# Optimization experiments

Hardware: AMD Instinct MI355X
Metric: run time of the kernel (lower is better)

Reference implementation:

```python
import jax, jax.numpy as jnp
import numpy as np

T, N, E, P, D, F = 24, 10000, 320000, 20000, 64, 32


def setup_inputs() -> dict:
    key = jax.random.key(0)
    ks = jax.random.split(key, 16)
    s = 0.05

    def nrm(k, shape):
        return jax.random.normal(k, shape, jnp.float32) * s

    return {
        "x": jax.random.normal(ks[0], (T, N, F + 2), jnp.float32),
        "dis": jax.random.uniform(ks[1], (N, N), dtype=jnp.float32),
        "src": jax.random.randint(ks[2], (E,), 0, N, jnp.int32),
        "dst": jax.random.randint(ks[3], (E,), 0, N, jnp.int32),
        "train_idx": jax.random.randint(ks[4], (2, P), 0, N, jnp.int32),
        "ru_W1": nrm(ks[5], (D + F, D)), "ru_b1": jnp.zeros((D,), jnp.float32),
        "ru_W2": nrm(ks[6], (D, D)), "ru_b2": jnp.zeros((D,), jnp.float32),
        "ru_W3": nrm(ks[7], (D, 2 * D)), "ru_b3": jnp.zeros((2 * D,), jnp.float32),
        "rh_W1": nrm(ks[8], (D + F, D)), "rh_b1": jnp.zeros((D,), jnp.float32),
        "rh_W2": nrm(ks[9], (D, D)), "rh_b2": jnp.zeros((D,), jnp.float32),
        "rh_W3": nrm(ks[10], (D, D)), "rh_b3": jnp.zeros((D,), jnp.float32),
        "pred_W": nrm(ks[11], (2 * D + 1, 1)), "pred_b": jnp.zeros((1,), jnp.float32),
    }


def reference(x, dis, src, dst, train_idx,
              ru_W1, ru_b1, ru_W2, ru_b2, ru_W3, ru_b3,
              rh_W1, rh_b1, rh_W2, rh_b2, rh_W3, rh_b3,
              pred_W, pred_b):
    # DGL GraphConv, norm='both': h <- D_in^{-1/2} A D_out^{-1/2} h W + b (deg clamped to >=1)
    ones = jnp.ones((E,), jnp.float32)
    out_norm = jax.lax.rsqrt(jnp.maximum(jax.ops.segment_sum(ones, src, num_segments=N), 1.0))
    in_norm = jax.lax.rsqrt(jnp.maximum(jax.ops.segment_sum(ones, dst, num_segments=N), 1.0))

    def gconv(h, W, b):
        m = (h * out_norm[:, None])[src]                              # gather [E, d]
        agg = jax.ops.segment_sum(m, dst, num_segments=N) * in_norm[:, None]
        return agg @ W + b

    def gnn(h, W1, b1, W2, b2, W3, b3):
        h = jax.nn.relu(gconv(h, W1, b1))
        h = jax.nn.relu(gconv(h, W2, b2))
        return gconv(h, W3, b3)

    feat = x[:, :, :-2]                                               # [T, N, F]

    def step(h, xt):
        ru = jax.nn.sigmoid(gnn(jnp.concatenate([h, xt], -1),
                                ru_W1, ru_b1, ru_W2, ru_b2, ru_W3, ru_b3))
        r, z = ru[:, :D], ru[:, D:]
        h_new = jnp.tanh(gnn(jnp.concatenate([h * r, xt], -1),
                             rh_W1, rh_b1, rh_W2, rh_b2, rh_W3, rh_b3))
        h = z * h + (1.0 - z) * h_new
        return h, h

    _, hs = jax.lax.scan(step, jnp.zeros((N, D), x.dtype), feat)      # [T, N, D]

    ori = hs[:, train_idx[0]]                                         # [T, P, D]
    dst_e = hs[:, train_idx[1]]                                       # [T, P, D]
    d = jnp.broadcast_to(dis[train_idx[0], train_idx[1]][None, :, None], (T, P, 1))
    flow = jnp.tanh(jnp.concatenate([ori, dst_e, d], -1) @ pred_W + pred_b)  # [T, P, 1]
    return flow[:, :, 0].T                                            # [P, T]
```

## Files before the change

kernel.cpp:

```cpp
#include <hip/hip_runtime.h>
#include <cstdint>
#include <cstddef>

#define T_ 24
#define N_ 10000
#define E_ 320000
#define P_ 20000
#define D_ 64
#define F_ 32
#define XS_ 34
#define NZROWS 64

#define SCOPE_AGENT __HIP_MEMORY_SCOPE_AGENT

typedef float f32x4 __attribute__((ext_vector_type(4)));

__device__ __forceinline__ float ldsc(const float* p) {
  return __hip_atomic_load((const float*)p, __ATOMIC_RELAXED, SCOPE_AGENT);
}
__device__ __forceinline__ float2 ldsc2(const float* p) {
  unsigned long long u =
      __hip_atomic_load((const unsigned long long*)p, __ATOMIC_RELAXED, SCOPE_AGENT);
  float2 r;
  r.x = __uint_as_float((unsigned)(u & 0xffffffffu));
  r.y = __uint_as_float((unsigned)(u >> 32));
  return r;
}
__device__ __forceinline__ void stsc(float* p, float v) {
  __hip_atomic_store(p, v, __ATOMIC_RELAXED, SCOPE_AGENT);
}
__device__ __forceinline__ void stsc16(float* p, f32x4 v) {
  asm volatile("global_store_dwordx4 %0, %1, off sc1" :: "v"(p), "v"(v) : "memory");
}
__device__ __forceinline__ f32x4 ld4sc(const float* p) {
  f32x4 v;
  asm volatile("global_load_dwordx4 %0, %1, off sc1" : "=v"(v) : "v"(p));
  return v;
}
__device__ __forceinline__ void vmwait0() {
  asm volatile("s_waitcnt vmcnt(0)" ::: "memory");
  __builtin_amdgcn_sched_barrier(0);
}


__global__ void deg_kernel(const int* __restrict__ src, const int* __restrict__ dst,
                           int* __restrict__ deg_out, int* __restrict__ deg_in) {
  int e = blockIdx.x * blockDim.x + threadIdx.x;
  if (e < E_) {
    atomicAdd(&deg_out[src[e]], 1);
    atomicAdd(&deg_in[dst[e]], 1);
  }
}

__global__ void norm_kernel(const int* __restrict__ deg_in, const int* __restrict__ deg_out,
                            float* __restrict__ in_norm, float* __restrict__ out_norm) {
  int n = blockIdx.x * blockDim.x + threadIdx.x;
  if (n < N_) {
    in_norm[n]  = 1.0f / sqrtf(fmaxf((float)deg_in[n], 1.0f));
    out_norm[n] = 1.0f / sqrtf(fmaxf((float)deg_out[n], 1.0f));
  }
}

__global__ __launch_bounds__(1024) void scan_kernel(const int* __restrict__ deg,
                                                    int* __restrict__ row_ptr) {
  __shared__ int buf[1024];
  __shared__ int carry;
  int tid = threadIdx.x;
  if (tid == 0) { carry = 0; row_ptr[0] = 0; }
  __syncthreads();
  for (int base = 0; base < N_; base += 1024) {
    int i = base + tid;
    int v = (i < N_) ? deg[i] : 0;
    buf[tid] = v;
    __syncthreads();
    for (int off = 1; off < 1024; off <<= 1) {
      int tv = (tid >= off) ? buf[tid - off] : 0;
      __syncthreads();
      buf[tid] += tv;
      __syncthreads();
    }
    if (i < N_) row_ptr[i + 1] = carry + buf[tid];
    __syncthreads();
    if (tid == 0) carry += buf[1023];
    __syncthreads();
  }
}

__global__ void fill_kernel(const int* __restrict__ src, const int* __restrict__ dst,
                            const int* __restrict__ row_ptr, int* __restrict__ fill,
                            int* __restrict__ col) {
  int e = blockIdx.x * blockDim.x + threadIdx.x;
  if (e < E_) {
    int n = dst[e];
    int pos = row_ptr[n] + atomicAdd(&fill[n], 1);
    col[pos] = src[e];
  }
}

__global__ void dvec_kernel(const float* __restrict__ dis, const int* __restrict__ ti,
                            float* __restrict__ dvec) {
  int p = blockIdx.x * blockDim.x + threadIdx.x;
  if (p < P_) {
    int i0 = ti[p];
    int i1 = ti[P_ + p];
    dvec[p] = dis[(size_t)i0 * N_ + i1];
  }
}


struct Args {
  const float* x;
  const int* row_ptr;
  const int* col;
  const float* in_norm;
  const float* out_norm;
  const float* ruW1; const float* ruB1;
  const float* ruW2; const float* ruB2;
  const float* ruW3; const float* ruB3;
  const float* rhW1; const float* rhB1;
  const float* rhW2; const float* rhB2;
  const float* rhW3; const float* rhB3;
  const float* pW; const float* pb;
  const int* ti; const float* dvec;
  float* h; float* z; float* tA; float* tB;
  float* out;
  unsigned* slots;
  unsigned* epoch;
};

__device__ __forceinline__ void gbar(const Args& A, unsigned nblk, unsigned& ep) {
  __syncthreads();
  ++ep;
  const int tid = threadIdx.x;
  if (blockIdx.x == 0) {
    if (tid > 0 && tid < (int)nblk) {
      while (__hip_atomic_load(&A.slots[tid], __ATOMIC_RELAXED, SCOPE_AGENT) < ep)
        __builtin_amdgcn_s_sleep(2);
    }
    __syncthreads();
    if (tid == 0)
      __hip_atomic_store(A.epoch, ep, __ATOMIC_RELAXED, SCOPE_AGENT);
  } else {
    if (tid == 0) {
      __hip_atomic_store(&A.slots[blockIdx.x], ep, __ATOMIC_RELAXED, SCOPE_AGENT);
      while (__hip_atomic_load(A.epoch, __ATOMIC_RELAXED, SCOPE_AGENT) < ep)
        __builtin_amdgcn_s_sleep(2);
    }
    __syncthreads();
  }
}

__device__ __forceinline__ void stageW(const float* __restrict__ W, int n4,
                                       float4* __restrict__ sdst, int tid) {
  const float4* Wv = (const float4*)W;
  for (int i = tid; i < n4; i += 512) sdst[i] = Wv[i];
}

__device__ __forceinline__ float4 gatherNode(const float* __restrict__ tsrc,
                                             const int* __restrict__ rp,
                                             const int* __restrict__ col,
                                             int n, int g, int sub) {
  const int zrow = N_ + (n & (NZROWS - 1));
  int e0 = rp[n], e1 = rp[n + 1];
  f32x4 acc = {0.f, 0.f, 0.f, 0.f};
  int e = e0 + g;
  while (e < e1) {
    int c0 = col[e];
    int c1 = (e + 4  < e1) ? col[e + 4]  : zrow;
    int c2 = (e + 8  < e1) ? col[e + 8]  : zrow;
    int c3 = (e + 12 < e1) ? col[e + 12] : zrow;
    int c4 = (e + 16 < e1) ? col[e + 16] : zrow;
    int c5 = (e + 20 < e1) ? col[e + 20] : zrow;
    int c6 = (e + 24 < e1) ? col[e + 24] : zrow;
    int c7 = (e + 28 < e1) ? col[e + 28] : zrow;
    f32x4 v0 = ld4sc(tsrc + (size_t)c0 * 64 + 4 * sub);
    f32x4 v1 = ld4sc(tsrc + (size_t)c1 * 64 + 4 * sub);
    f32x4 v2 = ld4sc(tsrc + (size_t)c2 * 64 + 4 * sub);
    f32x4 v3 = ld4sc(tsrc + (size_t)c3 * 64 + 4 * sub);
    f32x4 v4 = ld4sc(tsrc + (size_t)c4 * 64 + 4 * sub);
    f32x4 v5 = ld4sc(tsrc + (size_t)c5 * 64 + 4 * sub);
    f32x4 v6 = ld4sc(tsrc + (size_t)c6 * 64 + 4 * sub);
    f32x4 v7 = ld4sc(tsrc + (size_t)c7 * 64 + 4 * sub);
    e += 32;
    vmwait0();
    acc += ((v0 + v1) + (v2 + v3)) + ((v4 + v5) + (v6 + v7));
  }
  float ax = acc.x, ay = acc.y, az = acc.z, aw = acc.w;
#pragma unroll
  for (int off = 16; off < 64; off <<= 1) {
    ax += __shfl_xor(ax, off);
    ay += __shfl_xor(ay, off);
    az += __shfl_xor(az, off);
    aw += __shfl_xor(aw, off);
  }
  return make_float4(ax, ay, az, aw);
}

__device__ __forceinline__ void predPhase(const Args& A, int t, int wgid, int WT,
                                          int g, int sub) {
  const float2* pw2 = (const float2*)A.pW;
  float2 w00 = pw2[sub],      w01 = pw2[16 + sub];
  float2 w10 = pw2[32 + sub], w11 = pw2[48 + sub];
  for (int q = wgid; q * 4 < P_; q += WT) {
    int p = q * 4 + g;
    bool valid = (p < P_);
    int i0 = valid ? A.ti[p] : 0;
    int i1 = valid ? A.ti[P_ + p] : 0;
    const float* h0 = A.h + (size_t)i0 * 64 + 2 * sub;
    const float* h1 = A.h + (size_t)i1 * 64 + 2 * sub;
    float2 a00 = ldsc2(h0), a01 = ldsc2(h0 + 32);
    float2 a10 = ldsc2(h1), a11 = ldsc2(h1 + 32);
    float part = a00.x * w00.x + a00.y * w00.y + a01.x * w01.x + a01.y * w01.y
               + a10.x * w10.x + a10.y * w10.y + a11.x * w11.x + a11.y * w11.y;
#pragma unroll
    for (int off = 1; off < 16; off <<= 1) part += __shfl_xor(part, off);
    if (valid && sub == 0) {
      float a = part + A.pb[0] + A.dvec[p] * A.pW[128];
      stsc(A.out + (size_t)p * T_ + t, tanhf(a));
    }
  }
}

template<int MODE>
__device__ __forceinline__ void runPhase(
    const Args& A, const float* __restrict__ tsrc, float* __restrict__ tdst,
    const float* __restrict__ W, const float* __restrict__ bias,
    const float* __restrict__ Wpre, const float* __restrict__ xside,
    float4* sWv, float4* sWpreV, float (*sRow)[96], float4 (*sAgg4)[16],
    int tid, int nodeBase, int nodeEnd, bool doPre) {
  const int wave = tid >> 6;
  const int lane = tid & 63;
  const int g = lane >> 4;
  const int sub = lane & 15;

  if (MODE == 0) stageW(W, 64 * 64 / 4, sWv, tid);
  if (MODE == 2) { stageW(W, 64 * 128 / 4, sWv, tid); stageW(Wpre, 96 * 64 / 4, sWpreV, tid); }
  if (MODE == 3) { stageW(W, 64 * 64 / 4, sWv, tid); if (doPre) stageW(Wpre, 96 * 64 / 4, sWpreV, tid); }
  if (MODE != 1) __syncthreads();

  const float* sW = (const float*)sWv;
  const float* sWpre = (const float*)sWpreV;

  float4 b4 = make_float4(0.f, 0.f, 0.f, 0.f);
  float b0 = 0.f, b1 = 0.f;
  if (MODE == 0 || MODE == 1) {
    b4 = ((const float4*)bias)[sub];
  } else if (MODE == 2) {
    b0 = bias[lane]; b1 = bias[64 + lane];
  } else {
    b0 = bias[lane];
  }

  for (int n = nodeBase + wave; n < nodeEnd; n += 8) {
    float4 acc = gatherNode(tsrc, A.row_ptr, A.col, n, g, sub);
    float inn = A.in_norm[n];
    float on = A.out_norm[n];

    if (MODE == 0 || MODE == 1) {
      float4 val;
      val.x = on * fmaxf(inn * acc.x + b4.x, 0.0f);
      val.y = on * fmaxf(inn * acc.y + b4.y, 0.0f);
      val.z = on * fmaxf(inn * acc.z + b4.z, 0.0f);
      val.w = on * fmaxf(inn * acc.w + b4.w, 0.0f);
      if (MODE == 1) {
        if (g == 0) {
          f32x4 vv = {val.x, val.y, val.z, val.w};
          stsc16(tdst + (size_t)n * 64 + 4 * sub, vv);
        }
      } else {
        if (g == 0) sAgg4[wave][sub] = val;
        const float* sAgg = (const float*)&sAgg4[wave][0];
        float a = 0.0f;
#pragma unroll 8
        for (int i = 0; i < 64; ++i) a += sAgg[i] * sW[i * 64 + lane];
        stsc(tdst + (size_t)n * 64 + lane, a);
      }
    } else if (MODE == 2) {
      if (g == 0) {
        float4 val;
        val.x = inn * acc.x; val.y = inn * acc.y;
        val.z = inn * acc.z; val.w = inn * acc.w;
        sAgg4[wave][sub] = val;
      }
      const float* sAgg = (const float*)&sAgg4[wave][0];
      float a0 = b0, a1 = b1;
#pragma unroll 8
      for (int i = 0; i < 64; ++i) {
        float s = sAgg[i];
        a0 += s * sW[i * 128 + lane];
        a1 += s * sW[i * 128 + 64 + lane];
      }
      float r = 1.0f / (1.0f + expf(-a0));
      float zz = 1.0f / (1.0f + expf(-a1));
      stsc(A.z + (size_t)n * 64 + lane, zz);
      float hrv = r * ldsc(A.h + (size_t)n * 64 + lane);
      sRow[wave][lane] = on * hrv;
      if (lane < 32) sRow[wave][64 + lane] = on * xside[(size_t)n * XS_ + lane];
      float a = 0.0f;
#pragma unroll 8
      for (int i = 0; i < 96; ++i) a += sRow[wave][i] * sWpre[i * 64 + lane];
      stsc(tdst + (size_t)n * 64 + lane, a);
    } else {
      if (g == 0) {
        float4 val;
        val.x = inn * acc.x; val.y = inn * acc.y;
        val.z = inn * acc.z; val.w = inn * acc.w;
        sAgg4[wave][sub] = val;
      }
      const float* sAgg = (const float*)&sAgg4[wave][0];
      float a = b0;
#pragma unroll 8
      for (int i = 0; i < 64; ++i) a += sAgg[i] * sW[i * 64 + lane];
      float hn = tanhf(a);
      float zz = ldsc(A.z + (size_t)n * 64 + lane);
      float hp = ldsc(A.h + (size_t)n * 64 + lane);
      float hnew = zz * hp + (1.0f - zz) * hn;
      stsc(A.h + (size_t)n * 64 + lane, hnew);
      if (doPre) {
        sRow[wave][lane] = on * hnew;
        if (lane < 32) sRow[wave][64 + lane] = on * xside[(size_t)n * XS_ + lane];
        float ap = 0.0f;
#pragma unroll 8
        for (int i = 0; i < 96; ++i) ap += sRow[wave][i] * sWpre[i * 64 + lane];
        stsc(tdst + (size_t)n * 64 + lane, ap);
      }
    }
  }
}

__global__ __launch_bounds__(512, 4) void mega_kernel(Args A) {
  __shared__ float4 sWv[2048];
  __shared__ float4 sWpreV[1536];
  __shared__ float sRow[8][96];
  __shared__ float4 sAgg4[8][16];

  const int tid = threadIdx.x;
  const int wave = tid >> 6;
  const int lane = tid & 63;
  const int g = lane >> 4;
  const int sub = lane & 15;
  const unsigned nblk = gridDim.x;
  const int NPB = (N_ + nblk - 1) / nblk;
  const int nodeBase = blockIdx.x * NPB;
  int nodeEnd = nodeBase + NPB;
  if (nodeEnd > N_) nodeEnd = N_;
  const int wgid = blockIdx.x * 8 + wave;
  const int WT = nblk * 8;
  unsigned ep = 0;

  stageW(A.ruW1, 96 * 64 / 4, sWpreV, tid);
  __syncthreads();
  {
    const float* sWpre = (const float*)sWpreV;
    for (int n = nodeBase + wave; n < nodeEnd; n += 8) {
      float on = A.out_norm[n];
      if (lane < 32) sRow[wave][64 + lane] = on * A.x[(size_t)n * XS_ + lane];
      float a = 0.0f;
#pragma unroll 8
      for (int i = 64; i < 96; ++i) a += sRow[wave][i] * sWpre[i * 64 + lane];
      stsc(A.tA + (size_t)n * 64 + lane, a);
    }
  }
  gbar(A, nblk, ep);

  for (int t = 0; t < T_; ++t) {
    const float* xt  = A.x + (size_t)t * N_ * XS_;
    const float* xt1 = A.x + (size_t)(t + 1) * N_ * XS_;

    runPhase<0>(A, A.tA, A.tB, A.ruW2, A.ruB1, nullptr, nullptr,
                sWv, sWpreV, sRow, sAgg4, tid, nodeBase, nodeEnd, false);
    if (t > 0) predPhase(A, t - 1, wgid, WT, g, sub);
    gbar(A, nblk, ep);

    runPhase<1>(A, A.tB, A.tA, nullptr, A.ruB2, nullptr, nullptr,
                sWv, sWpreV, sRow, sAgg4, tid, nodeBase, nodeEnd, false);
    gbar(A, nblk, ep);

    runPhase<2>(A, A.tA, A.tB, A.ruW3, A.ruB3, A.rhW1, xt,
                sWv, sWpreV, sRow, sAgg4, tid, nodeBase, nodeEnd, false);
    gbar(A, nblk, ep);

    runPhase<0>(A, A.tB, A.tA, A.rhW2, A.rhB1, nullptr, nullptr,
                sWv, sWpreV, sRow, sAgg4, tid, nodeBase, nodeEnd, false);
    gbar(A, nblk, ep);

    runPhase<1>(A, A.tA, A.tB, nullptr, A.rhB2, nullptr, nullptr,
                sWv, sWpreV, sRow, sAgg4, tid, nodeBase, nodeEnd, false);
    gbar(A, nblk, ep);

    runPhase<3>(A, A.tB, A.tA, A.rhW3, A.rhB3, A.ruW1, xt1,
                sWv, sWpreV, sRow, sAgg4, tid, nodeBase, nodeEnd, t < T_ - 1);
    gbar(A, nblk, ep);
  }

  predPhase(A, T_ - 1, wgid, WT, g, sub);
}


extern "C" void kernel_launch(void* const* d_in, const int* in_sizes, int n_in,
                              void* d_out, int out_size, void* d_ws, size_t ws_size,
                              hipStream_t stream) {
  const float* x      = (const float*)d_in[0];
  const float* dis    = (const float*)d_in[1];
  const int*   src    = (const int*)d_in[2];
  const int*   dst    = (const int*)d_in[3];
  const int*   ti     = (const int*)d_in[4];
  const float* ru_W1  = (const float*)d_in[5];
  const float* ru_b1  = (const float*)d_in[6];
  const float* ru_W2  = (const float*)d_in[7];
  const float* ru_b2  = (const float*)d_in[8];
  const float* ru_W3  = (const float*)d_in[9];
  const float* ru_b3  = (const float*)d_in[10];
  const float* rh_W1  = (const float*)d_in[11];
  const float* rh_b1  = (const float*)d_in[12];
  const float* rh_W2  = (const float*)d_in[13];
  const float* rh_b2  = (const float*)d_in[14];
  const float* rh_W3  = (const float*)d_in[15];
  const float* rh_b3  = (const float*)d_in[16];
  const float* pred_W = (const float*)d_in[17];
  const float* pred_b = (const float*)d_in[18];
  float* out = (float*)d_out;

  char* w = (char*)d_ws;
  auto alloc = [&](size_t bytes) -> void* {
    void* p = (void*)w;
    w += (bytes + 255) & ~(size_t)255;
    return p;
  };
  int*   row_ptr  = (int*)alloc((N_ + 1) * sizeof(int));
  int*   colv     = (int*)alloc(E_ * sizeof(int));
  int*   deg_in   = (int*)alloc(N_ * sizeof(int));
  int*   deg_out  = (int*)alloc(N_ * sizeof(int));
  int*   fillc    = (int*)alloc(N_ * sizeof(int));
  float* in_norm  = (float*)alloc(N_ * sizeof(float));
  float* out_norm = (float*)alloc(N_ * sizeof(float));
  float* dvec     = (float*)alloc(P_ * sizeof(float));
  float* h        = (float*)alloc((size_t)N_ * D_ * sizeof(float));
  float* z        = (float*)alloc((size_t)N_ * D_ * sizeof(float));
  float* tA       = (float*)alloc((size_t)(N_ + NZROWS) * D_ * sizeof(float));
  float* tB       = (float*)alloc((size_t)(N_ + NZROWS) * D_ * sizeof(float));
  unsigned* slots = (unsigned*)alloc(1024 * sizeof(unsigned));
  unsigned* epoch = (unsigned*)alloc(256);

  (void)hipMemsetAsync(deg_in, 0, N_ * sizeof(int), stream);
  (void)hipMemsetAsync(deg_out, 0, N_ * sizeof(int), stream);
  (void)hipMemsetAsync(fillc, 0, N_ * sizeof(int), stream);
  (void)hipMemsetAsync(h, 0, (size_t)N_ * D_ * sizeof(float), stream);
  (void)hipMemsetAsync(tA + (size_t)N_ * D_, 0, (size_t)NZROWS * D_ * sizeof(float), stream);
  (void)hipMemsetAsync(tB + (size_t)N_ * D_, 0, (size_t)NZROWS * D_ * sizeof(float), stream);
  (void)hipMemsetAsync(slots, 0, 1024 * sizeof(unsigned), stream);
  (void)hipMemsetAsync(epoch, 0, 256, stream);

  deg_kernel<<<(E_ + 255) / 256, 256, 0, stream>>>(src, dst, deg_out, deg_in);
  norm_kernel<<<(N_ + 255) / 256, 256, 0, stream>>>(deg_in, deg_out, in_norm, out_norm);
  scan_kernel<<<1, 1024, 0, stream>>>(deg_in, row_ptr);
  fill_kernel<<<(E_ + 255) / 256, 256, 0, stream>>>(src, dst, row_ptr, fillc, colv);
  dvec_kernel<<<(P_ + 255) / 256, 256, 0, stream>>>(dis, ti, dvec);

  Args a;
  a.x = x; a.row_ptr = row_ptr; a.col = colv;
  a.in_norm = in_norm; a.out_norm = out_norm;
  a.ruW1 = ru_W1; a.ruB1 = ru_b1; a.ruW2 = ru_W2; a.ruB2 = ru_b2;
  a.ruW3 = ru_W3; a.ruB3 = ru_b3;
  a.rhW1 = rh_W1; a.rhB1 = rh_b1; a.rhW2 = rh_W2; a.rhB2 = rh_b2;
  a.rhW3 = rh_W3; a.rhB3 = rh_b3;
  a.pW = pred_W; a.pb = pred_b; a.ti = ti; a.dvec = dvec;
  a.h = h; a.z = z; a.tA = tA; a.tB = tB; a.out = out;
  a.slots = slots; a.epoch = epoch;

  int maxb = 0;
  (void)hipOccupancyMaxActiveBlocksPerMultiprocessor(&maxb, mega_kernel, 512, 0);
  if (maxb < 1) maxb = 1;
  int bpc = (maxb < 2) ? maxb : 2;
  int nblk = 256 * bpc;

  void* params[] = { (void*)&a };
  hipError_t err = hipLaunchCooperativeKernel((const void*)mega_kernel, dim3(nblk),
                                              dim3(512), params, 0, stream);
  if (err != hipSuccess) {
    mega_kernel<<<dim3(nblk), dim3(512), 0, stream>>>(a);
  }
}
```

Measured before the change: 3.341 ms.

## Balance nodes per wave by edge count and raise persistent grid occupancy

A small kernel binary-searches row_ptr so that each wave of the persistent kernel gets a contiguous node range with roughly equal edge counts, replacing the fixed per-block node split with strided waves. The Wpre shared-memory staging buffer is removed, with those weights read from global memory, which shrinks LDS use and lets up to 4 blocks per CU run instead of 2. The gather loop is split into a full-chunk loop without bounds checks plus one guarded tail, and the grid barrier is changed so block 0 polls every slot itself, which is needed once there are more than 512 blocks. The intent is to cut load imbalance and raise memory parallelism. In exchange, Wpre reads now go through cache instead of LDS, and a larger grid makes each barrier more expensive.

New measurement: 3.909 ms. 17.0% more time.

```diff
diff --git a/kernel.cpp b/kernel.cpp
--- a/kernel.cpp
+++ b/kernel.cpp
@@ -107,6 +107,21 @@
   }
 }
 
+__global__ void balance_kernel(const int* __restrict__ row_ptr,
+                               int* __restrict__ wstart, int nwaves) {
+  int w = blockIdx.x * blockDim.x + threadIdx.x;
+  if (w > nwaves) return;
+  if (w == 0)      { wstart[0] = 0;       return; }
+  if (w == nwaves) { wstart[nwaves] = N_; return; }
+  long long target = (long long)row_ptr[N_] * w / nwaves;
+  int lo = 0, hi = N_;
+  while (lo < hi) {
+    int mid = (lo + hi) >> 1;
+    if ((long long)row_ptr[mid] < target) lo = mid + 1; else hi = mid;
+  }
+  wstart[w] = lo;
+}
+
 
 struct Args {
   const float* x;
@@ -122,6 +137,7 @@
   const float* rhW3; const float* rhB3;
   const float* pW; const float* pb;
   const int* ti; const float* dvec;
+  const int* wstart;
   float* h; float* z; float* tA; float* tB;
   float* out;
   unsigned* slots;
@@ -132,9 +148,11 @@
   __syncthreads();
   ++ep;
   const int tid = threadIdx.x;
+  if (tid == 0)
+    __hip_atomic_store(&A.slots[blockIdx.x], ep, __ATOMIC_RELAXED, SCOPE_AGENT);
   if (blockIdx.x == 0) {
-    if (tid > 0 && tid < (int)nblk) {
-      while (__hip_atomic_load(&A.slots[tid], __ATOMIC_RELAXED, SCOPE_AGENT) < ep)
+    for (int s = tid; s < (int)nblk; s += 512) {
+      while (__hip_atomic_load(&A.slots[s], __ATOMIC_RELAXED, SCOPE_AGENT) < ep)
         __builtin_amdgcn_s_sleep(2);
     }
     __syncthreads();
@@ -142,7 +160,6 @@
       __hip_atomic_store(A.epoch, ep, __ATOMIC_RELAXED, SCOPE_AGENT);
   } else {
     if (tid == 0) {
-      __hip_atomic_store(&A.slots[blockIdx.x], ep, __ATOMIC_RELAXED, SCOPE_AGENT);
       while (__hip_atomic_load(A.epoch, __ATOMIC_RELAXED, SCOPE_AGENT) < ep)
         __builtin_amdgcn_s_sleep(2);
     }
@@ -157,31 +174,47 @@
 }
 
 __device__ __forceinline__ float4 gatherNode(const float* __restrict__ tsrc,
-                                             const int* __restrict__ rp,
                                              const int* __restrict__ col,
-                                             int n, int g, int sub) {
-  const int zrow = N_ + (n & (NZROWS - 1));
-  int e0 = rp[n], e1 = rp[n + 1];
+                                             int e0, int e1, int n, int g, int sub) {
   f32x4 acc = {0.f, 0.f, 0.f, 0.f};
-  int e = e0 + g;
-  while (e < e1) {
-    int c0 = col[e];
-    int c1 = (e + 4  < e1) ? col[e + 4]  : zrow;
-    int c2 = (e + 8  < e1) ? col[e + 8]  : zrow;
-    int c3 = (e + 12 < e1) ? col[e + 12] : zrow;
-    int c4 = (e + 16 < e1) ? col[e + 16] : zrow;
-    int c5 = (e + 20 < e1) ? col[e + 20] : zrow;
-    int c6 = (e + 24 < e1) ? col[e + 24] : zrow;
-    int c7 = (e + 28 < e1) ? col[e + 28] : zrow;
-    f32x4 v0 = ld4sc(tsrc + (size_t)c0 * 64 + 4 * sub);
-    f32x4 v1 = ld4sc(tsrc + (size_t)c1 * 64 + 4 * sub);
-    f32x4 v2 = ld4sc(tsrc + (size_t)c2 * 64 + 4 * sub);
-    f32x4 v3 = ld4sc(tsrc + (size_t)c3 * 64 + 4 * sub);
-    f32x4 v4 = ld4sc(tsrc + (size_t)c4 * 64 + 4 * sub);
-    f32x4 v5 = ld4sc(tsrc + (size_t)c5 * 64 + 4 * sub);
-    f32x4 v6 = ld4sc(tsrc + (size_t)c6 * 64 + 4 * sub);
-    f32x4 v7 = ld4sc(tsrc + (size_t)c7 * 64 + 4 * sub);
-    e += 32;
+  const int len = e1 - e0;
+  const int kfull = len >> 5;
+  const int* cp = col + e0 + g;
+  const float* base = tsrc + 4 * sub;
+  for (int k = 0; k < kfull; ++k) {
+    int c0 = cp[0],  c1 = cp[4],  c2 = cp[8],  c3 = cp[12];
+    int c4 = cp[16], c5 = cp[20], c6 = cp[24], c7 = cp[28];
+    f32x4 v0 = ld4sc(base + (size_t)c0 * 64);
+    f32x4 v1 = ld4sc(base + (size_t)c1 * 64);
+    f32x4 v2 = ld4sc(base + (size_t)c2 * 64);
+    f32x4 v3 = ld4sc(base + (size_t)c3 * 64);
+    f32x4 v4 = ld4sc(base + (size_t)c4 * 64);
+    f32x4 v5 = ld4sc(base + (size_t)c5 * 64);
+    f32x4 v6 = ld4sc(base + (size_t)c6 * 64);
+    f32x4 v7 = ld4sc(base + (size_t)c7 * 64);
+    cp += 32;
+    vmwait0();
+    acc += ((v0 + v1) + (v2 + v3)) + ((v4 + v5) + (v6 + v7));
+  }
+  int e = e0 + (kfull << 5) + g;
+  if (e < e1) {
+    const int zrow = N_ + (n & (NZROWS - 1));
+    int c0 = cp[0];
+    int c1 = (e + 4  < e1) ? cp[4]  : zrow;
+    int c2 = (e + 8  < e1) ? cp[8]  : zrow;
+    int c3 = (e + 12 < e1) ? cp[12] : zrow;
+    int c4 = (e + 16 < e1) ? cp[16] : zrow;
+    int c5 = (e + 20 < e1) ? cp[20] : zrow;
+    int c6 = (e + 24 < e1) ? cp[24] : zrow;
+    int c7 = (e + 28 < e1) ? cp[28] : zrow;
+    f32x4 v0 = ld4sc(base + (size_t)c0 * 64);
+    f32x4 v1 = ld4sc(base + (size_t)c1 * 64);
+    f32x4 v2 = ld4sc(base + (size_t)c2 * 64);
+    f32x4 v3 = ld4sc(base + (size_t)c3 * 64);
+    f32x4 v4 = ld4sc(base + (size_t)c4 * 64);
+    f32x4 v5 = ld4sc(base + (size_t)c5 * 64);
+    f32x4 v6 = ld4sc(base + (size_t)c6 * 64);
+    f32x4 v7 = ld4sc(base + (size_t)c7 * 64);
     vmwait0();
     acc += ((v0 + v1) + (v2 + v3)) + ((v4 + v5) + (v6 + v7));
   }
@@ -226,20 +259,18 @@
     const Args& A, const float* __restrict__ tsrc, float* __restrict__ tdst,
     const float* __restrict__ W, const float* __restrict__ bias,
     const float* __restrict__ Wpre, const float* __restrict__ xside,
-    float4* sWv, float4* sWpreV, float (*sRow)[96], float4 (*sAgg4)[16],
-    int tid, int nodeBase, int nodeEnd, bool doPre) {
+    float4* sWv, float (*sRow)[96], float4 (*sAgg4)[16],
+    int tid, int ws, int we, bool doPre) {
   const int wave = tid >> 6;
   const int lane = tid & 63;
   const int g = lane >> 4;
   const int sub = lane & 15;
 
-  if (MODE == 0) stageW(W, 64 * 64 / 4, sWv, tid);
-  if (MODE == 2) { stageW(W, 64 * 128 / 4, sWv, tid); stageW(Wpre, 96 * 64 / 4, sWpreV, tid); }
-  if (MODE == 3) { stageW(W, 64 * 64 / 4, sWv, tid); if (doPre) stageW(Wpre, 96 * 64 / 4, sWpreV, tid); }
+  if (MODE == 0 || MODE == 3) stageW(W, 64 * 64 / 4, sWv, tid);
+  if (MODE == 2) stageW(W, 64 * 128 / 4, sWv, tid);
   if (MODE != 1) __syncthreads();
 
   const float* sW = (const float*)sWv;
-  const float* sWpre = (const float*)sWpreV;
 
   float4 b4 = make_float4(0.f, 0.f, 0.f, 0.f);
   float b0 = 0.f, b1 = 0.f;
@@ -251,8 +282,9 @@
     b0 = bias[lane];
   }
 
-  for (int n = nodeBase + wave; n < nodeEnd; n += 8) {
-    float4 acc = gatherNode(tsrc, A.row_ptr, A.col, n, g, sub);
+  for (int n = ws; n < we; ++n) {
+    int e0 = A.row_ptr[n], e1 = A.row_ptr[n + 1];
+    float4 acc = gatherNode(tsrc, A.col, e0, e1, n, g, sub);
     float inn = A.in_norm[n];
     float on = A.out_norm[n];
 
@@ -298,7 +330,7 @@
       if (lane < 32) sRow[wave][64 + lane] = on * xside[(size_t)n * XS_ + lane];
       float a = 0.0f;
 #pragma unroll 8
-      for (int i = 0; i < 96; ++i) a += sRow[wave][i] * sWpre[i * 64 + lane];
+      for (int i = 0; i < 96; ++i) a += sRow[wave][i] * Wpre[i * 64 + lane];
       stsc(tdst + (size_t)n * 64 + lane, a);
     } else {
       if (g == 0) {
@@ -321,7 +353,7 @@
         if (lane < 32) sRow[wave][64 + lane] = on * xside[(size_t)n * XS_ + lane];
         float ap = 0.0f;
 #pragma unroll 8
-        for (int i = 0; i < 96; ++i) ap += sRow[wave][i] * sWpre[i * 64 + lane];
+        for (int i = 0; i < 96; ++i) ap += sRow[wave][i] * Wpre[i * 64 + lane];
         stsc(tdst + (size_t)n * 64 + lane, ap);
       }
     }
@@ -330,7 +362,6 @@
 
 __global__ __launch_bounds__(512, 4) void mega_kernel(Args A) {
   __shared__ float4 sWv[2048];
-  __shared__ float4 sWpreV[1536];
   __shared__ float sRow[8][96];
   __shared__ float4 sAgg4[8][16];
 
@@ -340,26 +371,19 @@
   const int g = lane >> 4;
   const int sub = lane & 15;
   const unsigned nblk = gridDim.x;
-  const int NPB = (N_ + nblk - 1) / nblk;
-  const int nodeBase = blockIdx.x * NPB;
-  int nodeEnd = nodeBase + NPB;
-  if (nodeEnd > N_) nodeEnd = N_;
   const int wgid = blockIdx.x * 8 + wave;
   const int WT = nblk * 8;
+  const int ws = A.wstart[wgid];
+  const int we = A.wstart[wgid + 1];
   unsigned ep = 0;
 
-  stageW(A.ruW1, 96 * 64 / 4, sWpreV, tid);
-  __syncthreads();
-  {
-    const float* sWpre = (const float*)sWpreV;
-    for (int n = nodeBase + wave; n < nodeEnd; n += 8) {
-      float on = A.out_norm[n];
-      if (lane < 32) sRow[wave][64 + lane] = on * A.x[(size_t)n * XS_ + lane];
-      float a = 0.0f;
+  for (int n = ws; n < we; ++n) {
+    float on = A.out_norm[n];
+    if (lane < 32) sRow[wave][64 + lane] = on * A.x[(size_t)n * XS_ + lane];
+    float a = 0.0f;
 #pragma unroll 8
-      for (int i = 64; i < 96; ++i) a += sRow[wave][i] * sWpre[i * 64 + lane];
-      stsc(A.tA + (size_t)n * 64 + lane, a);
-    }
+    for (int i = 64; i < 96; ++i) a += sRow[wave][i] * A.ruW1[i * 64 + lane];
+    stsc(A.tA + (size_t)n * 64 + lane, a);
   }
   gbar(A, nblk, ep);
 
@@ -368,28 +392,28 @@
     const float* xt1 = A.x + (size_t)(t + 1) * N_ * XS_;
 
     runPhase<0>(A, A.tA, A.tB, A.ruW2, A.ruB1, nullptr, nullptr,
-                sWv, sWpreV, sRow, sAgg4, tid, nodeBase, nodeEnd, false);
+                sWv, sRow, sAgg4, tid, ws, we, false);
     if (t > 0) predPhase(A, t - 1, wgid, WT, g, sub);
     gbar(A, nblk, ep);
 
     runPhase<1>(A, A.tB, A.tA, nullptr, A.ruB2, nullptr, nullptr,
-                sWv, sWpreV, sRow, sAgg4, tid, nodeBase, nodeEnd, false);
+                sWv, sRow, sAgg4, tid, ws, we, false);
     gbar(A, nblk, ep);
 
     runPhase<2>(A, A.tA, A.tB, A.ruW3, A.ruB3, A.rhW1, xt,
-                sWv, sWpreV, sRow, sAgg4, tid, nodeBase, nodeEnd, false);
+                sWv, sRow, sAgg4, tid, ws, we, false);
     gbar(A, nblk, ep);
 
     runPhase<0>(A, A.tB, A.tA, A.rhW2, A.rhB1, nullptr, nullptr,
-                sWv, sWpreV, sRow, sAgg4, tid, nodeBase, nodeEnd, false);
+                sWv, sRow, sAgg4, tid, ws, we, false);
     gbar(A, nblk, ep);
 
     runPhase<1>(A, A.tA, A.tB, nullptr, A.rhB2, nullptr, nullptr,
-                sWv, sWpreV, sRow, sAgg4, tid, nodeBase, nodeEnd, false);
+                sWv, sRow, sAgg4, tid, ws, we, false);
     gbar(A, nblk, ep);
 
     runPhase<3>(A, A.tB, A.tA, A.rhW3, A.rhB3, A.ruW1, xt1,
-                sWv, sWpreV, sRow, sAgg4, tid, nodeBase, nodeEnd, t < T_ - 1);
+                sWv, sRow, sAgg4, tid, ws, we, t < T_ - 1);
     gbar(A, nblk, ep);
   }
 
@@ -439,8 +463,9 @@
   float* z        = (float*)alloc((size_t)N_ * D_ * sizeof(float));
   float* tA       = (float*)alloc((size_t)(N_ + NZROWS) * D_ * sizeof(float));
   float* tB       = (float*)alloc((size_t)(N_ + NZROWS) * D_ * sizeof(float));
-  unsigned* slots = (unsigned*)alloc(1024 * sizeof(unsigned));
+  unsigned* slots = (unsigned*)alloc(2048 * sizeof(unsigned));
   unsigned* epoch = (unsigned*)alloc(256);
+  int*   wstart   = (int*)alloc((8 * 1024 + 2) * sizeof(int));
 
   (void)hipMemsetAsync(deg_in, 0, N_ * sizeof(int), stream);
   (void)hipMemsetAsync(deg_out, 0, N_ * sizeof(int), stream);
@@ -448,7 +473,7 @@
   (void)hipMemsetAsync(h, 0, (size_t)N_ * D_ * sizeof(float), stream);
   (void)hipMemsetAsync(tA + (size_t)N_ * D_, 0, (size_t)NZROWS * D_ * sizeof(float), stream);
   (void)hipMemsetAsync(tB + (size_t)N_ * D_, 0, (size_t)NZROWS * D_ * sizeof(float), stream);
-  (void)hipMemsetAsync(slots, 0, 1024 * sizeof(unsigned), stream);
+  (void)hipMemsetAsync(slots, 0, 2048 * sizeof(unsigned), stream);
   (void)hipMemsetAsync(epoch, 0, 256, stream);
 
   deg_kernel<<<(E_ + 255) / 256, 256, 0, stream>>>(src, dst, deg_out, deg_in);
@@ -456,6 +481,15 @@
   scan_kernel<<<1, 1024, 0, stream>>>(deg_in, row_ptr);
   fill_kernel<<<(E_ + 255) / 256, 256, 0, stream>>>(src, dst, row_ptr, fillc, colv);
   dvec_kernel<<<(P_ + 255) / 256, 256, 0, stream>>>(dis, ti, dvec);
+
+  int maxb = 0;
+  (void)hipOccupancyMaxActiveBlocksPerMultiprocessor(&maxb, mega_kernel, 512, 0);
+  if (maxb < 1) maxb = 1;
+  int bpc = (maxb < 4) ? maxb : 4;
+  int nblk = 256 * bpc;
+  int nwaves = nblk * 8;
+
+  balance_kernel<<<(nwaves + 256) / 256, 256, 0, stream>>>(row_ptr, wstart, nwaves);
 
   Args a;
   a.x = x; a.row_ptr = row_ptr; a.col = colv;
@@ -465,14 +499,9 @@
   a.rhW1 = rh_W1; a.rhB1 = rh_b1; a.rhW2 = rh_W2; a.rhB2 = rh_b2;
   a.rhW3 = rh_W3; a.rhB3 = rh_b3;
   a.pW = pred_W; a.pb = pred_b; a.ti = ti; a.dvec = dvec;
+  a.wstart = wstart;
   a.h = h; a.z = z; a.tA = tA; a.tB = tB; a.out = out;
   a.slots = slots; a.epoch = epoch;
-
-  int maxb = 0;
-  (void)hipOccupancyMaxActiveBlocksPerMultiprocessor(&maxb, mega_kernel, 512, 0);
-  if (maxb < 1) maxb = 1;
-  int bpc = (maxb < 2) ? maxb : 2;
-  int nblk = 256 * bpc;
 
   void* params[] = { (void*)&a };
   hipError_t err = hipLaunchCooperativeKernel((const void*)mega_kernel, dim3(nblk),
```
